# Optimization experiments

Measured on AMD Instinct MI355X. Metric: run time of the kernel, lower is better.

The kernel has to match this reference:

```python
import jax, jax.numpy as jnp
import numpy as np

B, T, D = 2, 2048, 2048
NH, NKV, HD = 16, 4, 128
ROPE_DIMS = 64
EPS = 1e-6


def _rope_tables(t, rd, base=10000.0):
    # rd dims are rotated as two halves of size rd//2; cos/sin are [T, rd]
    inv_freq = 1.0 / (base ** (jnp.arange(0, rd // 2, dtype=jnp.float32) * 2.0 / rd))
    ang = jnp.arange(t, dtype=jnp.float32)[:, None] * inv_freq[None, :]  # [T, rd//2]
    ang = jnp.concatenate([ang, ang], axis=-1)  # [T, rd]
    return jnp.cos(ang), jnp.sin(ang)


def setup_inputs() -> dict:
    key = jax.random.key(0)
    ks = jax.random.split(key, 6)
    x = jax.random.normal(ks[0], (B, T, D), dtype=jnp.float32)
    cos, sin = _rope_tables(T, ROPE_DIMS)
    s = 1.0 / np.sqrt(D)
    wq = jax.random.normal(ks[1], (NH * HD, D), dtype=jnp.float32) * s
    wk = jax.random.normal(ks[2], (NKV * HD, D), dtype=jnp.float32) * s
    wv = jax.random.normal(ks[3], (NKV * HD, D), dtype=jnp.float32) * s
    wo = jax.random.normal(ks[4], (NH * HD, D), dtype=jnp.float32).T * s  # [NH*HD, D] -> stored torch-style below
    wo = jax.random.normal(ks[5], (D, NH * HD), dtype=jnp.float32) * s  # torch Linear weight [out,in]
    w_norm = jnp.ones((D,), dtype=jnp.float32)
    return {"x": x, "cos": cos, "sin": sin, "w_norm": w_norm, "wq": wq,
            "wk": wk, "wv": wv, "wo": wo, "rope_dims": ROPE_DIMS, "use_xsa": 1}


def _rmsnorm(x, w, eps=EPS):
    ms = jnp.mean(x * x, axis=-1, keepdims=True)
    return x * jax.lax.rsqrt(ms + eps) * w


def _rotate_half(x):
    x1, x2 = jnp.split(x, 2, axis=-1)
    return jnp.concatenate([-x2, x1], axis=-1)


def _apply_partial_rope(q, k, cos, sin, rd):
    # q: [B,T,NH,HD], k: [B,T,NKV,HD]; cos/sin: [T,rd]
    c = cos[None, :, None, :]
    s = sin[None, :, None, :]
    def rot(t):
        tr, tp = t[..., :rd], t[..., rd:]
        tr = tr * c + _rotate_half(tr) * s
        return jnp.concatenate([tr, tp], axis=-1)
    return rot(q), rot(k)


def reference(x, cos, sin, w_norm, wq, wk, wv, wo, rope_dims, use_xsa):
    b, t, d = x.shape
    group = NH // NKV
    h = _rmsnorm(x, w_norm)
    q = jnp.einsum('btd,ed->bte', h, wq).reshape(b, t, NH, HD)
    k = jnp.einsum('btd,ed->bte', h, wk).reshape(b, t, NKV, HD)
    v = jnp.einsum('btd,ed->bte', h, wv).reshape(b, t, NKV, HD)
    q, k = _apply_partial_rope(q, k, cos, sin, rope_dims)
    # GQA: repeat KV heads across groups, then [B,H,T,HD]
    k = jnp.repeat(k, group, axis=2).transpose(0, 2, 1, 3)
    v = jnp.repeat(v, group, axis=2).transpose(0, 2, 1, 3)
    q = q.transpose(0, 2, 1, 3)
    scores = jnp.einsum('bhqd,bhkd->bhqk', q, k) / np.sqrt(HD)
    causal = jnp.tril(jnp.ones((t, t), dtype=bool))
    scores = jnp.where(causal[None, None], scores, jnp.finfo(scores.dtype).min)
    attn = jax.nn.softmax(scores, axis=-1)
    out = jnp.einsum('bhqk,bhkd->bhqd', attn, v)
    if use_xsa:
        dot = jnp.sum(out * v, axis=-1, keepdims=True)
        vns = jnp.sum(v * v, axis=-1, keepdims=True) + 1e-6
        out = out - dot * v / vns
    out = out.transpose(0, 2, 1, 3).reshape(b, t, NH * HD)
    return jnp.einsum('bte,de->btd', out, wo)
```

## Files before the change

### kernel.cpp

```cpp
#include <hip/hip_runtime.h>
#include <hip/hip_bf16.h>
#include <stdint.h>

#define B_ 2
#define T_ 2048
#define D_ 2048
#define NH_ 16
#define NKV_ 4
#define HD_ 128
#define EQ_ (NH_*HD_)
#define EKV_ (NKV_*HD_)
#define EQKV_ (EQ_ + 2*EKV_)
#define KOFF_ EQ_
#define VOFF_ (EQ_ + EKV_)

typedef __attribute__((ext_vector_type(8))) short short8;
typedef __attribute__((ext_vector_type(4))) short short4x;
typedef __attribute__((ext_vector_type(4))) float floatx4;

static __device__ __forceinline__ ushort f2bf(float f) {
  uint u = __builtin_bit_cast(uint, f);
  u = (u + 0x7fffu + ((u >> 16) & 1u)) >> 16;
  return (ushort)u;
}
static __device__ __forceinline__ float bf2f(ushort u) {
  return __builtin_bit_cast(float, ((uint)u) << 16);
}

#define S1_ (EQ_*D_)
#define S2_ (S1_ + EKV_*D_)
#define S3_ (S2_ + EKV_*D_)
#define S4_ (S3_ + D_*EQ_)
__global__ __launch_bounds__(256) void cvt4_k(const float* __restrict__ wq,
                                              const float* __restrict__ wk,
                                              const float* __restrict__ wv,
                                              const float* __restrict__ wo,
                                              ushort* __restrict__ wqkv,
                                              ushort* __restrict__ wob) {
  int i = (blockIdx.x * 256 + threadIdx.x) * 2;
  const float* s;
  ushort* d;
  int j;
  if (i < S1_)      { s = wq; d = wqkv + i; j = i; }
  else if (i < S2_) { s = wk; d = wqkv + i; j = i - S1_; }
  else if (i < S3_) { s = wv; d = wqkv + i; j = i - S2_; }
  else              { s = wo; d = wob + (i - S3_); j = i - S3_; }
  float2 f = *(const float2*)&s[j];
  ushort2 u;
  u.x = f2bf(f.x);
  u.y = f2bf(f.y);
  *(ushort2*)d = u;
}

__global__ __launch_bounds__(256) void rmsnorm_k(const float* __restrict__ x,
                                                 const float* __restrict__ wn,
                                                 ushort* __restrict__ hb) {
  const int row = blockIdx.x, tid = threadIdx.x;
  const int w = tid >> 6, lane = tid & 63;
  const float* xr = x + (size_t)row * D_;
  float v[8];
  float4 a = *(const float4*)&xr[tid * 8];
  float4 b = *(const float4*)&xr[tid * 8 + 4];
  v[0] = a.x; v[1] = a.y; v[2] = a.z; v[3] = a.w;
  v[4] = b.x; v[5] = b.y; v[6] = b.z; v[7] = b.w;
  float ss = 0.f;
#pragma unroll
  for (int i = 0; i < 8; i++) ss += v[i] * v[i];
  for (int m = 32; m; m >>= 1) ss += __shfl_xor(ss, m);
  __shared__ float red[4];
  if (lane == 0) red[w] = ss;
  __syncthreads();
  float tot = red[0] + red[1] + red[2] + red[3];
  float sc = rsqrtf(tot * (1.f / D_) + 1e-6f);
  short8 st;
#pragma unroll
  for (int i = 0; i < 8; i++) st[i] = (short)f2bf(v[i] * sc * wn[tid * 8 + i]);
  *(short8*)(hb + (size_t)row * D_ + tid * 8) = st;
}

template <bool OUT_F32>
__global__ __launch_bounds__(256) void gemm_bt(const ushort* __restrict__ A,
                                               const ushort* __restrict__ W,
                                               void* __restrict__ Cp,
                                               int M, int N, int K) {
  __shared__ __align__(16) ushort lA[128 * 64];
  __shared__ __align__(16) ushort lB[128 * 64];
  const int tid = threadIdx.x;
  const int w = tid >> 6, lane = tid & 63;
  const int bm = blockIdx.y, bn = blockIdx.x;
  const int wm = w >> 1, wn = w & 1;
  const int l15 = lane & 15, l4 = lane >> 4;
  const int swz = (l15 & 7) * 8;

  floatx4 acc[4][4];
#pragma unroll
  for (int m = 0; m < 4; m++)
#pragma unroll
    for (int n = 0; n < 4; n++) acc[m][n] = floatx4{0.f, 0.f, 0.f, 0.f};

  for (int k0 = 0; k0 < K; k0 += 64) {
#pragma unroll
    for (int r = 0; r < 4; ++r) {
      int c = r * 256 + tid;
      int row = c >> 3, cw = c & 7;
      int scol = k0 + ((cw ^ (row & 7)) << 3);
      const ushort* ga = A + (size_t)(bm * 128 + row) * K + scol;
      __builtin_amdgcn_global_load_lds(
          (const __attribute__((address_space(1))) void*)ga,
          (__attribute__((address_space(3))) void*)&lA[c * 8], 16, 0, 0);
      const ushort* gb = W + (size_t)(bn * 128 + row) * K + scol;
      __builtin_amdgcn_global_load_lds(
          (const __attribute__((address_space(1))) void*)gb,
          (__attribute__((address_space(3))) void*)&lB[c * 8], 16, 0, 0);
    }
    __syncthreads();
#pragma unroll
    for (int kk = 0; kk < 2; kk++) {
      short8 av[4], bv[4];
      int co = (kk * 32 + l4 * 8) ^ swz;
#pragma unroll
      for (int m = 0; m < 4; m++)
        av[m] = *(const short8*)&lA[(wm * 64 + m * 16 + l15) * 64 + co];
#pragma unroll
      for (int n = 0; n < 4; n++)
        bv[n] = *(const short8*)&lB[(wn * 64 + n * 16 + l15) * 64 + co];
#pragma unroll
      for (int m = 0; m < 4; m++)
#pragma unroll
        for (int n = 0; n < 4; n++)
          acc[m][n] = __builtin_amdgcn_mfma_f32_16x16x32_bf16(av[m], bv[n], acc[m][n], 0, 0, 0);
    }
    __syncthreads();
  }

  if (OUT_F32) {
    float* C = (float*)Cp;
#pragma unroll
    for (int m = 0; m < 4; m++)
#pragma unroll
      for (int n = 0; n < 4; n++)
#pragma unroll
        for (int j = 0; j < 4; j++) {
          int row = bm * 128 + wm * 64 + m * 16 + l4 * 4 + j;
          int col = bn * 128 + wn * 64 + n * 16 + l15;
          C[(size_t)row * N + col] = acc[m][n][j];
        }
  } else {
    ushort* C = (ushort*)Cp;
#pragma unroll
    for (int m = 0; m < 4; m++)
#pragma unroll
      for (int n = 0; n < 4; n++)
#pragma unroll
        for (int j = 0; j < 4; j++) {
          int row = bm * 128 + wm * 64 + m * 16 + l4 * 4 + j;
          int col = bn * 128 + wn * 64 + n * 16 + l15;
          C[(size_t)row * N + col] = f2bf(acc[m][n][j]);
        }
  }
}

__global__ __launch_bounds__(256) void rope_k(ushort* __restrict__ X,
                                              const float* __restrict__ cosT,
                                              const float* __restrict__ sinT,
                                              int rd) {
  int idx = blockIdx.x * 256 + threadIdx.x;
  int half = rd >> 1;
  int total = B_ * T_ * (NH_ + NKV_) * half;
  if (idx >= total) return;
  int i = idx % half;
  int r2 = idx / half;
  int hh = r2 % (NH_ + NKV_);
  int row = r2 / (NH_ + NKV_);
  int t = row % T_;
  int col = (hh < NH_) ? hh * HD_ : KOFF_ + (hh - NH_) * HD_;
  ushort* p = X + (size_t)row * EQKV_ + col;
  float x0 = bf2f(p[i]), x1 = bf2f(p[i + half]);
  float c0 = cosT[t * rd + i], s0 = sinT[t * rd + i];
  float c1 = cosT[t * rd + i + half], s1 = sinT[t * rd + i + half];
  p[i] = f2bf(x0 * c0 - x1 * s0);
  p[i + half] = f2bf(x1 * c1 + x0 * s1);
}

__global__ __launch_bounds__(256) void vtr_k(const ushort* __restrict__ V,
                                             int vstride,
                                             ushort* __restrict__ Vt) {
  __shared__ ushort tile[32][34];
  const int tb = blockIdx.x, eb = blockIdx.y, b = blockIdx.z;
  const int tid = threadIdx.x;
  const int r = tid >> 3, c4 = (tid & 7) * 4;
  short4x in = *(const short4x*)&V[((size_t)(b * T_ + tb * 32 + r)) * vstride + eb * 32 + c4];
#pragma unroll
  for (int i = 0; i < 4; i++) tile[r][c4 + i] = (ushort)in[i];
  __syncthreads();
  short4x out;
#pragma unroll
  for (int i = 0; i < 4; i++) out[i] = (short)tile[c4 + i][r];
  *(short4x*)&Vt[((size_t)(b * EKV_ + eb * 32 + r)) * T_ + tb * 32 + c4] = out;
}

__global__ __launch_bounds__(256, 2) void attn_k(const ushort* __restrict__ QKV,
                                                 const ushort* __restrict__ Vt,
                                                 float* __restrict__ O) {
  __shared__ __align__(16) ushort Klds[2][8192];
  __shared__ __align__(16) ushort Vlds[2][8192];
  __shared__ __align__(16) char P_lds[4 * 2048];
  const int tid = threadIdx.x, w = tid >> 6, lane = tid & 63;
  const int l15 = lane & 15, l4 = lane >> 4;
  const int h = blockIdx.y, b = blockIdx.z, kv = h >> 2;
  const int px = blockIdx.x;
  const int wbase = w * 2048;
  const float c_ = 0.12752626f;
  const float THR_ = 90.5f;

  const ushort* Kh = QKV + KOFF_ + (size_t)b * T_ * EQKV_ + kv * HD_;
  const ushort* Vth = Vt + ((size_t)(b * EKV_ + kv * HD_)) * T_;

  auto stageK = [&](int buf, int kvb) {
#pragma unroll
    for (int i = 0; i < 4; i++) {
      int q = i * 256 + tid;
      int r = q >> 4, cw = q & 15;
      const ushort* src = Kh + (size_t)(kvb + r) * EQKV_ + ((cw ^ (r & 7)) << 3);
      __builtin_amdgcn_global_load_lds(
          (const __attribute__((address_space(1))) void*)src,
          (__attribute__((address_space(3))) void*)&Klds[buf][q * 8], 16, 0, 0);
    }
  };
  auto stageV = [&](int buf, int kvb) {
#pragma unroll
    for (int i = 0; i < 4; i++) {
      int q = i * 256 + tid;
      int d = q >> 3, cw = q & 7;
      const ushort* src = Vth + (size_t)d * T_ + kvb + ((cw ^ (d & 7)) << 3);
      __builtin_amdgcn_global_load_lds(
          (const __attribute__((address_space(1))) void*)src,
          (__attribute__((address_space(3))) void*)&Vlds[buf][q * 8], 16, 0, 0);
    }
  };

  for (int hh = 0; hh < 2; hh++) {
    const int qb = hh ? (31 - px) : px;
    const int nt = qb + 1;
    const int qbase = qb * 64 + w * 16;

    short8 qf[4];
#pragma unroll
    for (int kk = 0; kk < 4; kk++)
      qf[kk] = *(const short8*)&QKV[(size_t)(b * T_ + qbase + l15) * EQKV_ + h * HD_ + kk * 32 + l4 * 8];

    floatx4 acc_o[8];
#pragma unroll
    for (int nn = 0; nn < 8; nn++) acc_o[nn] = floatx4{0.f, 0.f, 0.f, 0.f};
    float mj[4] = {-1e30f, -1e30f, -1e30f, -1e30f};
    float lj[4] = {0.f, 0.f, 0.f, 0.f};

    stageV(0, 0);
    stageK(0, 0);
    __syncthreads();
    int cur = 0;

    for (int t = 0; t < nt; t++) {
      const int kvb = t * 64;
      if (t + 1 < nt) {
        stageV(cur ^ 1, kvb + 64);
        stageK(cur ^ 1, kvb + 64);
      }

      floatx4 s[4];
#pragma unroll
      for (int n = 0; n < 4; n++) s[n] = floatx4{0.f, 0.f, 0.f, 0.f};
      __builtin_amdgcn_s_setprio(1);
#pragma unroll
      for (int n = 0; n < 4; n++) {
        int row = n * 16 + l15;
#pragma unroll
        for (int kk = 0; kk < 4; kk++) {
          int bc = (kk * 64 + l4 * 16) ^ ((row & 7) << 4);
          short8 kf = *(const short8*)&Klds[cur][row * 128 + (bc >> 1)];
          s[n] = __builtin_amdgcn_mfma_f32_16x16x32_bf16(qf[kk], kf, s[n], 0, 0, 0);
        }
      }
      __builtin_amdgcn_s_setprio(0);

      float pm[4] = {-1e30f, -1e30f, -1e30f, -1e30f};
      if (t == nt - 1) {
#pragma unroll
        for (int n = 0; n < 4; n++)
#pragma unroll
          for (int j = 0; j < 4; j++) {
            int col = kvb + n * 16 + l15;
            int row = qbase + l4 * 4 + j;
            float sv = (col <= row) ? s[n][j] : -1e30f;
            s[n][j] = sv;
            pm[j] = fmaxf(pm[j], sv);
          }
      } else {
#pragma unroll
        for (int n = 0; n < 4; n++)
#pragma unroll
          for (int j = 0; j < 4; j++) pm[j] = fmaxf(pm[j], s[n][j]);
      }
#pragma unroll
      for (int j = 0; j < 4; j++) {
        pm[j] = fmaxf(pm[j], __shfl_xor(pm[j], 1));
        pm[j] = fmaxf(pm[j], __shfl_xor(pm[j], 2));
        pm[j] = fmaxf(pm[j], __shfl_xor(pm[j], 4));
        pm[j] = fmaxf(pm[j], __shfl_xor(pm[j], 8));
      }
      float worst = fmaxf(fmaxf(pm[0] - mj[0], pm[1] - mj[1]),
                          fmaxf(pm[2] - mj[2], pm[3] - mj[3]));
      if (!__all(worst <= THR_)) {
#pragma unroll
        for (int j = 0; j < 4; j++) {
          float mn = fmaxf(mj[j], pm[j]);
          float sc = exp2f((mj[j] - mn) * c_);
          mj[j] = mn;
          lj[j] *= sc;
#pragma unroll
          for (int nn = 0; nn < 8; nn++) acc_o[nn][j] *= sc;
        }
      }
      float ps[4] = {0.f, 0.f, 0.f, 0.f};
#pragma unroll
      for (int n = 0; n < 4; n++)
#pragma unroll
        for (int j = 0; j < 4; j++) {
          float p = exp2f((s[n][j] - mj[j]) * c_);
          ps[j] += p;
          int r = l4 * 4 + j;
          int byteoff = ((r * 128 + (n * 16 + l15) * 2) ^ ((r & 7) << 4));
          *(ushort*)(P_lds + wbase + byteoff) = f2bf(p);
        }
#pragma unroll
      for (int j = 0; j < 4; j++) {
        ps[j] += __shfl_xor(ps[j], 1);
        ps[j] += __shfl_xor(ps[j], 2);
        ps[j] += __shfl_xor(ps[j], 4);
        ps[j] += __shfl_xor(ps[j], 8);
        lj[j] += ps[j];
      }

      __builtin_amdgcn_s_setprio(1);
#pragma unroll
      for (int kk = 0; kk < 2; kk++) {
        int rbyte = ((l15 * 128 + kk * 64 + l4 * 16) ^ ((l15 & 7) << 4));
        short8 pa = *(const short8*)(P_lds + wbase + rbyte);
#pragma unroll
        for (int n = 0; n < 8; n++) {
          int d = n * 16 + l15;
          int bc = (kk * 64 + l4 * 16) ^ ((d & 7) << 4);
          short8 vf = *(const short8*)&Vlds[cur][d * 64 + (bc >> 1)];
          acc_o[n] = __builtin_amdgcn_mfma_f32_16x16x32_bf16(pa, vf, acc_o[n], 0, 0, 0);
        }
      }
      __builtin_amdgcn_s_setprio(0);
      __syncthreads();
      cur ^= 1;
    }

#pragma unroll
    for (int j = 0; j < 4; j++) {
      float inv = 1.f / lj[j];
#pragma unroll
      for (int n = 0; n < 8; n++)
        O[(size_t)((b * NH_ + h) * T_ + qbase + l4 * 4 + j) * HD_ + n * 16 + l15] = acc_o[n][j] * inv;
    }
  }
}

__global__ __launch_bounds__(256) void xsa_k(const float* __restrict__ O,
                                             const ushort* __restrict__ QKV,
                                             const int* __restrict__ flag,
                                             ushort* __restrict__ att) {
  int w = threadIdx.x >> 6, lane = threadIdx.x & 63;
  int idx = blockIdx.x * 4 + w;
  int t = idx % T_;
  int bh = idx / T_;
  int h = bh % NH_;
  int b = bh / NH_;
  const float* o = O + (size_t)idx * HD_;
  const ushort* v = QKV + VOFF_ + (size_t)(b * T_ + t) * EQKV_ + (h >> 2) * HD_;
  float o0 = o[lane], o1 = o[lane + 64];
  float v0 = bf2f(v[lane]), v1 = bf2f(v[lane + 64]);
  float dot = o0 * v0 + o1 * v1;
  float vns = v0 * v0 + v1 * v1;
  for (int m = 32; m; m >>= 1) {
    dot += __shfl_xor(dot, m);
    vns += __shfl_xor(vns, m);
  }
  if (*flag) {
    float f = dot / (vns + 1e-6f);
    o0 -= f * v0;
    o1 -= f * v1;
  }
  ushort* ap = att + (size_t)(b * T_ + t) * EQ_ + h * HD_;
  ap[lane] = f2bf(o0);
  ap[lane + 64] = f2bf(o1);
}

extern "C" void kernel_launch(void* const* d_in, const int* in_sizes, int n_in,
                              void* d_out, int out_size, void* d_ws, size_t ws_size,
                              hipStream_t stream) {
  const float* x    = (const float*)d_in[0];
  const float* cosT = (const float*)d_in[1];
  const float* sinT = (const float*)d_in[2];
  const float* wn   = (const float*)d_in[3];
  const float* wq   = (const float*)d_in[4];
  const float* wk   = (const float*)d_in[5];
  const float* wv   = (const float*)d_in[6];
  const float* wo   = (const float*)d_in[7];
  const int* use_xsa = (const int*)d_in[9];
  int rd = in_sizes[1] / T_;

  char* ws = (char*)d_ws;
  size_t off = 0;
  auto alloc = [&](size_t bytes) {
    char* p = ws + off;
    off += (bytes + 255) & ~(size_t)255;
    return p;
  };
  ushort* h_b    = (ushort*)alloc((size_t)B_ * T_ * D_ * 2);
  ushort* qkv_b  = (ushort*)alloc((size_t)B_ * T_ * EQKV_ * 2);
  ushort* wqkv_b = (ushort*)alloc((size_t)EQKV_ * D_ * 2);
  ushort* wo_b   = (ushort*)alloc((size_t)D_ * EQ_ * 2);
  float*  o_f    = (float*)alloc((size_t)B_ * NH_ * T_ * HD_ * 4);
  ushort* att_b  = h_b;
  ushort* vt_b   = wqkv_b;

  cvt4_k<<<S4_ / 512, 256, 0, stream>>>(wq, wk, wv, wo, wqkv_b, wo_b);
  rmsnorm_k<<<B_ * T_, 256, 0, stream>>>(x, wn, h_b);

  dim3 gqkv(EQKV_ / 128, B_ * T_ / 128);
  gemm_bt<false><<<gqkv, 256, 0, stream>>>(h_b, wqkv_b, qkv_b, B_ * T_, EQKV_, D_);

  dim3 gvt(T_ / 32, EKV_ / 32, B_);
  vtr_k<<<gvt, 256, 0, stream>>>(qkv_b + VOFF_, EQKV_, vt_b);

  int half = rd / 2;
  int tot = B_ * T_ * (NH_ + NKV_) * half;
  rope_k<<<(tot + 255) / 256, 256, 0, stream>>>(qkv_b, cosT, sinT, rd);

  dim3 ga(16, NH_, B_);
  attn_k<<<ga, 256, 0, stream>>>(qkv_b, vt_b, o_f);

  xsa_k<<<B_ * NH_ * T_ / 4, 256, 0, stream>>>(o_f, qkv_b, use_xsa, att_b);

  dim3 go(D_ / 128, B_ * T_ / 128);
  gemm_bt<true><<<go, 256, 0, stream>>>(att_b, wo_b, d_out, B_ * T_, D_, D_);
}
```

Measured before the change: 236.2 us.

## Fuse XSA projection into attention epilogue and streamline softmax inner loop

Folds the XSA subtraction and bf16 conversion into the attention kernel's epilogue, which removes the fp32 O buffer round-trip through global memory and one kernel launch. It also replaces the softmax exponent argument with a single FMA on a precomputed scaled max, and converts P to bf16 with plain round-half-up instead of round-to-nearest-even. The row-sum shuffle reduction now runs after the PV MFMAs so it can overlap with them, and the K/V staging addresses advance by pointer increments. The epilogue loads V per row with strided 2-byte reads and adds register pressure at a point where occupancy is bounded by launch bounds.

```diff
diff --git a/kernel.cpp b/kernel.cpp
--- a/kernel.cpp
+++ b/kernel.cpp
@@ -201,7 +201,8 @@
 
 __global__ __launch_bounds__(256, 2) void attn_k(const ushort* __restrict__ QKV,
                                                  const ushort* __restrict__ Vt,
-                                                 float* __restrict__ O) {
+                                                 const int* __restrict__ flag,
+                                                 ushort* __restrict__ att) {
   __shared__ __align__(16) ushort Klds[2][8192];
   __shared__ __align__(16) ushort Vlds[2][8192];
   __shared__ __align__(16) char P_lds[4 * 2048];
@@ -212,27 +213,28 @@
   const int wbase = w * 2048;
   const float c_ = 0.12752626f;
   const float THR_ = 90.5f;
+  const int flagv = *flag;
 
   const ushort* Kh = QKV + KOFF_ + (size_t)b * T_ * EQKV_ + kv * HD_;
   const ushort* Vth = Vt + ((size_t)(b * EKV_ + kv * HD_)) * T_;
 
-  auto stageK = [&](int buf, int kvb) {
+  auto stageK = [&](int buf, const ushort* kp) {
 #pragma unroll
     for (int i = 0; i < 4; i++) {
       int q = i * 256 + tid;
       int r = q >> 4, cw = q & 15;
-      const ushort* src = Kh + (size_t)(kvb + r) * EQKV_ + ((cw ^ (r & 7)) << 3);
+      const ushort* src = kp + (size_t)r * EQKV_ + ((cw ^ (r & 7)) << 3);
       __builtin_amdgcn_global_load_lds(
           (const __attribute__((address_space(1))) void*)src,
           (__attribute__((address_space(3))) void*)&Klds[buf][q * 8], 16, 0, 0);
     }
   };
-  auto stageV = [&](int buf, int kvb) {
+  auto stageV = [&](int buf, const ushort* vp) {
 #pragma unroll
     for (int i = 0; i < 4; i++) {
       int q = i * 256 + tid;
       int d = q >> 3, cw = q & 7;
-      const ushort* src = Vth + (size_t)d * T_ + kvb + ((cw ^ (d & 7)) << 3);
+      const ushort* src = vp + (size_t)d * T_ + ((cw ^ (d & 7)) << 3);
       __builtin_amdgcn_global_load_lds(
           (const __attribute__((address_space(1))) void*)src,
           (__attribute__((address_space(3))) void*)&Vlds[buf][q * 8], 16, 0, 0);
@@ -255,17 +257,20 @@
     float mj[4] = {-1e30f, -1e30f, -1e30f, -1e30f};
     float lj[4] = {0.f, 0.f, 0.f, 0.f};
 
-    stageV(0, 0);
-    stageK(0, 0);
+    const ushort* kp = Kh;
+    const ushort* vp = Vth;
+    stageV(0, vp);
+    stageK(0, kp);
     __syncthreads();
     int cur = 0;
 
     for (int t = 0; t < nt; t++) {
-      const int kvb = t * 64;
       if (t + 1 < nt) {
-        stageV(cur ^ 1, kvb + 64);
-        stageK(cur ^ 1, kvb + 64);
-      }
+        stageV(cur ^ 1, vp + 64);
+        stageK(cur ^ 1, kp + 64 * EQKV_);
+      }
+      kp += 64 * EQKV_;
+      vp += 64;
 
       floatx4 s[4];
 #pragma unroll
@@ -289,7 +294,7 @@
         for (int n = 0; n < 4; n++)
 #pragma unroll
           for (int j = 0; j < 4; j++) {
-            int col = kvb + n * 16 + l15;
+            int col = (nt - 1) * 64 + n * 16 + l15;
             int row = qbase + l4 * 4 + j;
             float sv = (col <= row) ? s[n][j] : -1e30f;
             s[n][j] = sv;
@@ -321,17 +326,36 @@
           for (int nn = 0; nn < 8; nn++) acc_o[nn][j] *= sc;
         }
       }
+      float mc[4];
+#pragma unroll
+      for (int j = 0; j < 4; j++) mc[j] = mj[j] * c_;
       float ps[4] = {0.f, 0.f, 0.f, 0.f};
 #pragma unroll
       for (int n = 0; n < 4; n++)
 #pragma unroll
         for (int j = 0; j < 4; j++) {
-          float p = exp2f((s[n][j] - mj[j]) * c_);
+          float p = exp2f(__builtin_fmaf(s[n][j], c_, -mc[j]));
           ps[j] += p;
+          uint pu = (__builtin_bit_cast(uint, p) + 0x8000u) >> 16;
           int r = l4 * 4 + j;
           int byteoff = ((r * 128 + (n * 16 + l15) * 2) ^ ((r & 7) << 4));
-          *(ushort*)(P_lds + wbase + byteoff) = f2bf(p);
-        }
+          *(ushort*)(P_lds + wbase + byteoff) = (ushort)pu;
+        }
+
+      __builtin_amdgcn_s_setprio(1);
+#pragma unroll
+      for (int kk = 0; kk < 2; kk++) {
+        int rbyte = ((l15 * 128 + kk * 64 + l4 * 16) ^ ((l15 & 7) << 4));
+        short8 pa = *(const short8*)(P_lds + wbase + rbyte);
+#pragma unroll
+        for (int n = 0; n < 8; n++) {
+          int d = n * 16 + l15;
+          int bc = (kk * 64 + l4 * 16) ^ ((d & 7) << 4);
+          short8 vf = *(const short8*)&Vlds[cur][d * 64 + (bc >> 1)];
+          acc_o[n] = __builtin_amdgcn_mfma_f32_16x16x32_bf16(pa, vf, acc_o[n], 0, 0, 0);
+        }
+      }
+      __builtin_amdgcn_s_setprio(0);
 #pragma unroll
       for (int j = 0; j < 4; j++) {
         ps[j] += __shfl_xor(ps[j], 1);
@@ -340,21 +364,6 @@
         ps[j] += __shfl_xor(ps[j], 8);
         lj[j] += ps[j];
       }
-
-      __builtin_amdgcn_s_setprio(1);
-#pragma unroll
-      for (int kk = 0; kk < 2; kk++) {
-        int rbyte = ((l15 * 128 + kk * 64 + l4 * 16) ^ ((l15 & 7) << 4));
-        short8 pa = *(const short8*)(P_lds + wbase + rbyte);
-#pragma unroll
-        for (int n = 0; n < 8; n++) {
-          int d = n * 16 + l15;
-          int bc = (kk * 64 + l4 * 16) ^ ((d & 7) << 4);
-          short8 vf = *(const short8*)&Vlds[cur][d * 64 + (bc >> 1)];
-          acc_o[n] = __builtin_amdgcn_mfma_f32_16x16x32_bf16(pa, vf, acc_o[n], 0, 0, 0);
-        }
-      }
-      __builtin_amdgcn_s_setprio(0);
       __syncthreads();
       cur ^= 1;
     }
@@ -362,41 +371,32 @@
 #pragma unroll
     for (int j = 0; j < 4; j++) {
       float inv = 1.f / lj[j];
-#pragma unroll
-      for (int n = 0; n < 8; n++)
-        O[(size_t)((b * NH_ + h) * T_ + qbase + l4 * 4 + j) * HD_ + n * 16 + l15] = acc_o[n][j] * inv;
+      int q = qbase + l4 * 4 + j;
+      const ushort* vq = QKV + VOFF_ + (size_t)(b * T_ + q) * EQKV_ + kv * HD_;
+      float ov[8], vv[8], dot = 0.f, vns = 0.f;
+#pragma unroll
+      for (int n = 0; n < 8; n++) {
+        float o = acc_o[n][j] * inv;
+        float v = bf2f(vq[n * 16 + l15]);
+        ov[n] = o;
+        vv[n] = v;
+        dot += o * v;
+        vns += v * v;
+      }
+      dot += __shfl_xor(dot, 1); vns += __shfl_xor(vns, 1);
+      dot += __shfl_xor(dot, 2); vns += __shfl_xor(vns, 2);
+      dot += __shfl_xor(dot, 4); vns += __shfl_xor(vns, 4);
+      dot += __shfl_xor(dot, 8); vns += __shfl_xor(vns, 8);
+      if (flagv) {
+        float f = dot / (vns + 1e-6f);
+#pragma unroll
+        for (int n = 0; n < 8; n++) ov[n] -= f * vv[n];
+      }
+      ushort* ap = att + (size_t)(b * T_ + q) * EQ_ + h * HD_;
+#pragma unroll
+      for (int n = 0; n < 8; n++) ap[n * 16 + l15] = f2bf(ov[n]);
     }
   }
-}
-
-__global__ __launch_bounds__(256) void xsa_k(const float* __restrict__ O,
-                                             const ushort* __restrict__ QKV,
-                                             const int* __restrict__ flag,
-                                             ushort* __restrict__ att) {
-  int w = threadIdx.x >> 6, lane = threadIdx.x & 63;
-  int idx = blockIdx.x * 4 + w;
-  int t = idx % T_;
-  int bh = idx / T_;
-  int h = bh % NH_;
-  int b = bh / NH_;
-  const float* o = O + (size_t)idx * HD_;
-  const ushort* v = QKV + VOFF_ + (size_t)(b * T_ + t) * EQKV_ + (h >> 2) * HD_;
-  float o0 = o[lane], o1 = o[lane + 64];
-  float v0 = bf2f(v[lane]), v1 = bf2f(v[lane + 64]);
-  float dot = o0 * v0 + o1 * v1;
-  float vns = v0 * v0 + v1 * v1;
-  for (int m = 32; m; m >>= 1) {
-    dot += __shfl_xor(dot, m);
-    vns += __shfl_xor(vns, m);
-  }
-  if (*flag) {
-    float f = dot / (vns + 1e-6f);
-    o0 -= f * v0;
-    o1 -= f * v1;
-  }
-  ushort* ap = att + (size_t)(b * T_ + t) * EQ_ + h * HD_;
-  ap[lane] = f2bf(o0);
-  ap[lane + 64] = f2bf(o1);
 }
 
 extern "C" void kernel_launch(void* const* d_in, const int* in_sizes, int n_in,
@@ -424,7 +424,6 @@
   ushort* qkv_b  = (ushort*)alloc((size_t)B_ * T_ * EQKV_ * 2);
   ushort* wqkv_b = (ushort*)alloc((size_t)EQKV_ * D_ * 2);
   ushort* wo_b   = (ushort*)alloc((size_t)D_ * EQ_ * 2);
-  float*  o_f    = (float*)alloc((size_t)B_ * NH_ * T_ * HD_ * 4);
   ushort* att_b  = h_b;
   ushort* vt_b   = wqkv_b;
 
@@ -442,9 +441,7 @@
   rope_k<<<(tot + 255) / 256, 256, 0, stream>>>(qkv_b, cosT, sinT, rd);
 
   dim3 ga(16, NH_, B_);
-  attn_k<<<ga, 256, 0, stream>>>(qkv_b, vt_b, o_f);
-
-  xsa_k<<<B_ * NH_ * T_ / 4, 256, 0, stream>>>(o_f, qkv_b, use_xsa, att_b);
+  attn_k<<<ga, 256, 0, stream>>>(qkv_b, vt_b, use_xsa, att_b);
 
   dim3 go(D_ / 128, B_ * T_ / 128);
   gemm_bt<true><<<go, 256, 0, stream>>>(att_b, wo_b, d_out, B_ * T_, D_, D_);
```

Result: faster. 225.1 us (-4.7%).
